# Performance work log

Measured on AMD Instinct MI355X. Metric: run time of the kernel, lower is better.

## Reference

```python
import jax, jax.numpy as jnp
import numpy as np
import math

DIM = 512
HID = 2048
BS, SLEN = 4, 4096


def _bayes_linear(x, mu, log_sigma, eps):
    # torchbnn BayesLinear: W = mu + exp(log_sigma) * eps; y = x @ W^T
    W = mu + jnp.exp(log_sigma) * eps
    return jnp.einsum('...i,oi->...o', x, W)


def setup_inputs() -> dict:
    key = jax.random.key(0)
    ks = jax.random.split(key, 20)
    d = {}
    d['x'] = jax.random.normal(ks[0], (BS, SLEN, DIM), dtype=jnp.float32)
    # causal additive mask, broadcast over batch
    causal = jnp.triu(jnp.full((SLEN, SLEN), -1e9, dtype=jnp.float32), k=1)
    d['mask'] = causal[None, :, :]
    shapes = {'wk': (DIM, DIM), 'wv': (DIM, DIM), 'wo': (DIM, DIM), 'w1': (HID, DIM), 'w2': (DIM, HID)}
    i = 1
    for name, shp in shapes.items():
        fan_in = shp[1]
        d[name + '_mu'] = jax.random.normal(ks[i], shp, dtype=jnp.float32) / np.sqrt(fan_in); i += 1
        d[name + '_ls'] = (-3.0 + 0.1 * jax.random.normal(ks[i], shp, dtype=jnp.float32)); i += 1
        d[name + '_eps'] = jax.random.normal(ks[i], shp, dtype=jnp.float32); i += 1
    return d


def reference(x, mask, wk_mu, wk_ls, wk_eps, wv_mu, wv_ls, wv_eps, wo_mu, wo_ls, wo_eps,
              w1_mu, w1_ls, w1_eps, w2_mu, w2_ls, w2_eps):
    dim = x.shape[-1]
    # attention: W_q is identity
    xq = x
    xk = _bayes_linear(x, wk_mu, wk_ls, wk_eps)
    xv = _bayes_linear(x, wv_mu, wv_ls, wv_eps)
    scores = jnp.einsum('bqd,bkd->bqk', xq, xk) / math.sqrt(dim) + mask
    attn = jax.nn.softmax(scores, axis=-1)
    h = jnp.einsum('bqk,bkd->bqd', attn, xv)
    h_attn = _bayes_linear(h, wo_mu, wo_ls, wo_eps)
    h_res = x + h_attn
    # FFN with ReLU
    ff = _bayes_linear(h_res, w1_mu, w1_ls, w1_eps)
    ff = jax.nn.relu(ff)
    ff = _bayes_linear(ff, w2_mu, w2_ls, w2_eps)
    return h_res + ff
```

## Files before the change

kernel.cpp:

```cpp
#include <hip/hip_runtime.h>
#include <hip/hip_bf16.h>

typedef __hip_bfloat16 bf16;
typedef __attribute__((ext_vector_type(8))) short short8;
typedef __attribute__((ext_vector_type(4))) float f32x4;

#define MFMA16(a,b,c) __builtin_amdgcn_mfma_f32_16x16x32_bf16(a,b,c,0,0,0)

__device__ __forceinline__ void gl_lds16(const void* g, void* l) {
  __builtin_amdgcn_global_load_lds(
      (const __attribute__((address_space(1))) void*)g,
      (__attribute__((address_space(3))) void*)l, 16, 0, 0);
}

__global__ __launch_bounds__(256) void prep_kernel(
    const float* __restrict__ x,
    const float* __restrict__ m0, const float* __restrict__ l0, const float* __restrict__ e0,
    const float* __restrict__ m1, const float* __restrict__ l1, const float* __restrict__ e1,
    const float* __restrict__ m2, const float* __restrict__ l2, const float* __restrict__ e2,
    const float* __restrict__ m3, const float* __restrict__ l3, const float* __restrict__ e3,
    const float* __restrict__ m4, const float* __restrict__ l4, const float* __restrict__ e4,
    bf16* __restrict__ xb, bf16* __restrict__ wts)
{
  long e = ((long)blockIdx.x * 256 + threadIdx.x) * 4;
  if (e < 8388608L) {
    float4 v = *(const float4*)(x + e);
    union { bf16 b[4]; short4 s; } u;
    u.b[0] = __float2bfloat16(v.x); u.b[1] = __float2bfloat16(v.y);
    u.b[2] = __float2bfloat16(v.z); u.b[3] = __float2bfloat16(v.w);
    *(short4*)(xb + e) = u.s;
  } else {
    long we = e - 8388608L;
    const float *mu, *ls, *ep; long off = we;
    if (we < 262144L)        { mu = m0; ls = l0; ep = e0; }
    else if (we < 524288L)   { mu = m1; ls = l1; ep = e1; off = we - 262144L; }
    else if (we < 786432L)   { mu = m2; ls = l2; ep = e2; off = we - 524288L; }
    else if (we < 1835008L)  { mu = m3; ls = l3; ep = e3; off = we - 786432L; }
    else                     { mu = m4; ls = l4; ep = e4; off = we - 1835008L; }
    float4 a = *(const float4*)(mu + off);
    float4 b = *(const float4*)(ls + off);
    float4 c = *(const float4*)(ep + off);
    union { bf16 w[4]; short4 s; } u;
    u.w[0] = __float2bfloat16(a.x + __expf(b.x) * c.x);
    u.w[1] = __float2bfloat16(a.y + __expf(b.y) * c.y);
    u.w[2] = __float2bfloat16(a.z + __expf(b.z) * c.z);
    u.w[3] = __float2bfloat16(a.w + __expf(b.w) * c.w);
    *(short4*)(wts + we) = u.s;
  }
}

template<int MODE>
__global__ __launch_bounds__(256, 2) void gemm_nt(
    const bf16* __restrict__ A, const bf16* __restrict__ B,
    const float* __restrict__ resid, float* __restrict__ outf,
    bf16* __restrict__ outb, int M, int N, int K)
{
  __shared__ bf16 As[128 * 64];
  __shared__ bf16 Bs[128 * 64];
  const int t = threadIdx.x, w = t >> 6, lane = t & 63;
  const int quad = lane >> 4, c16 = lane & 15;
  const int bm = blockIdx.x << 7, bn = blockIdx.y << 7;
  const int wr = (w >> 1) << 6, wc = (w & 1) << 6;

  f32x4 acc[4][4] = {};

  const int lh = lane >> 3, l8 = lane & 7;
  const int gcol = (l8 ^ lh) << 3;
  const bf16* Ab = A + (long)bm * K;
  const bf16* Bb = B + (long)bn * K;

  for (int k0 = 0; k0 < K; k0 += 64) {
    #pragma unroll
    for (int r2 = 0; r2 < 4; r2++) {
      const int R0 = r2 * 32 + w * 8;
      gl_lds16(Ab + (long)(R0 + lh) * K + k0 + gcol, (char*)As + R0 * 128);
      gl_lds16(Bb + (long)(R0 + lh) * K + k0 + gcol, (char*)Bs + R0 * 128);
    }
    __syncthreads();
    short8 a[2][4], b[2][4];
    const int sw = c16 & 7;
    #pragma unroll
    for (int i = 0; i < 4; i++) {
      const int ra = (wr + i * 16 + c16) * 64;
      const int rb = (wc + i * 16 + c16) * 64;
      a[0][i] = *(const short8*)(As + ra + ((quad ^ sw) << 3));
      a[1][i] = *(const short8*)(As + ra + (((quad + 4) ^ sw) << 3));
      b[0][i] = *(const short8*)(Bs + rb + ((quad ^ sw) << 3));
      b[1][i] = *(const short8*)(Bs + rb + (((quad + 4) ^ sw) << 3));
    }
    #pragma unroll
    for (int kk = 0; kk < 2; kk++)
      #pragma unroll
      for (int i = 0; i < 4; i++)
        #pragma unroll
        for (int j = 0; j < 4; j++)
          acc[i][j] = MFMA16(a[kk][i], b[kk][j], acc[i][j]);
    __syncthreads();
  }

  #pragma unroll
  for (int i = 0; i < 4; i++) {
    const int row = bm + wr + i * 16 + quad * 4;
    #pragma unroll
    for (int j = 0; j < 4; j++) {
      const int col = bn + wc + j * 16 + c16;
      #pragma unroll
      for (int r = 0; r < 4; r++) {
        float v = acc[i][j][r];
        if (MODE == 4) {
          int n = (row + r) & 31;
          long idx = (long)(row + r) * 512 + ((((col >> 3) ^ (n & 7)) << 3) | (col & 7));
          outb[idx] = __float2bfloat16(v);
        } else if (MODE == 5) {
          int g = row + r;
          int kvl = g & 31;
          long idx = (((long)(g >> 5)) << 14) + (long)col * 32 +
                     (((kvl >> 3) ^ ((col >> 1) & 3)) << 3) + (kvl & 7);
          outb[idx] = __float2bfloat16(v);
        } else {
          long idx = (long)(row + r) * N + col;
          if (MODE == 0) {
            outb[idx] = __float2bfloat16(v);
          } else if (MODE == 1) {
            float vv = v + resid[idx];
            outf[idx] = vv;
            outb[idx] = __float2bfloat16(vv);
          } else if (MODE == 2) {
            outb[idx] = __float2bfloat16(v > 0.f ? v : 0.f);
          } else {
            outf[idx] = v + resid[idx];
          }
        }
      }
    }
  }
}

__global__ __launch_bounds__(256, 2) void attn4_kernel(
    const bf16* __restrict__ xq, const bf16* __restrict__ xkS,
    const bf16* __restrict__ xvS, bf16* __restrict__ Opart,
    float* __restrict__ lsum)
{
  __shared__ bf16 Ks[32 * 512];
  __shared__ bf16 Vs[512 * 32];
  __shared__ bf16 Pb[4 * 512];

  const int t = threadIdx.x, w = t >> 6, lane = t & 63;
  const int quad = lane >> 4, c16 = lane & 15;
  const int n = blockIdx.x;
  const int B = n & 3, par = (n >> 2) & 3, i = n >> 4;
  const long boff = (long)B * (4096L * 512);
  const float scale = 0.04419417382415922f;
  const float FM = 30.0f;

  union { short8 s; short u[8]; } ones;
  #pragma unroll
  for (int k = 0; k < 8; k++) ones.u[k] = (short)0x3F80;

  for (int seg = 0; seg < 2; seg++) {
    const int qt = seg ? (63 - i) : i;
    const int T = 2 * (qt + 1);
    const int qb = qt << 6;

    short8 qf[16];
    {
      const bf16* qrow = xq + boff + (long)(qb + w * 16 + c16) * 512 + quad * 8;
      #pragma unroll
      for (int f = 0; f < 16; f++) qf[f] = *(const short8*)(qrow + f * 32);
    }

    f32x4 o[32];
    #pragma unroll
    for (int jj = 0; jj < 32; jj++) o[jj] = (f32x4){0.f, 0.f, 0.f, 0.f};
    f32x4 lacc = (f32x4){0.f, 0.f, 0.f, 0.f};

    for (int tile = par; tile < T; tile += 4) {
      const int kv0 = tile << 5;
      {
        const long tb = ((long)(B * 128 + tile)) << 14;
        const bf16* ks = xkS + tb + (w << 9) + (lane << 3);
        const bf16* vs = xvS + tb + (w << 9) + (lane << 3);
        char* kd = (char*)Ks + (w << 10);
        char* vd = (char*)Vs + (w << 10);
        #pragma unroll
        for (int r2 = 0; r2 < 8; r2++) {
          gl_lds16(ks + (r2 << 11), kd + (r2 << 12));
          gl_lds16(vs + (r2 << 11), vd + (r2 << 12));
        }
      }
      __syncthreads();

      f32x4 s0 = (f32x4){0.f, 0.f, 0.f, 0.f};
      f32x4 s1 = s0;
      const int n0 = c16, n1 = 16 + c16;
      const int sw0 = (c16 & 7) << 3;
      #pragma unroll
      for (int f = 0; f < 16; f++) {
        int cb = (f * 4 + quad) << 3;
        short8 b0 = *(const short8*)(Ks + n0 * 512 + (cb ^ sw0));
        short8 b1 = *(const short8*)(Ks + n1 * 512 + (cb ^ sw0));
        s0 = MFMA16(qf[f], b0, s0);
        s1 = MFMA16(qf[f], b1, s1);
      }

      bf16* Pw = Pb + (w << 9);
      {
        const int qr0 = qb + w * 16 + quad * 4;
        const bool need_mask = (kv0 + 32 > qb);
        #pragma unroll
        for (int r = 0; r < 4; r++) {
          float p0 = __expf(fmaf(s0[r], scale, -FM));
          float p1 = __expf(fmaf(s1[r], scale, -FM));
          if (need_mask) {
            if (kv0 + n0 > qr0 + r) p0 = 0.f;
            if (kv0 + n1 > qr0 + r) p1 = 0.f;
          }
          int pr = quad * 4 + r;
          int swp = (pr >> 1) & 3;
          Pw[pr * 32 + (((n0 >> 3) ^ swp) << 3) + (n0 & 7)] = __float2bfloat16(p0);
          Pw[pr * 32 + (((n1 >> 3) ^ swp) << 3) + (n1 & 7)] = __float2bfloat16(p1);
        }
      }
      short8 pa = *(const short8*)(Pw + c16 * 32 + ((quad ^ ((c16 >> 1) & 3)) << 3));
      lacc = MFMA16(pa, ones.s, lacc);
      #pragma unroll
      for (int jj = 0; jj < 32; jj++) {
        int d = jj * 16 + c16;
        short8 vb = *(const short8*)(Vs + d * 32 + ((quad ^ ((d >> 1) & 3)) << 3));
        o[jj] = MFMA16(pa, vb, o[jj]);
      }
      __syncthreads();
    }

    const int pidx = (B * 64 + qt) * 4 + par;
    {
      bf16* ob = Opart + ((long)pidx << 15) + (long)(w * 16 + quad * 4) * 512 + c16;
      #pragma unroll
      for (int r = 0; r < 4; r++) {
        #pragma unroll
        for (int jj = 0; jj < 32; jj++)
          ob[(long)r * 512 + jj * 16] = __float2bfloat16(o[jj][r]);
      }
      if (c16 == 0) {
        #pragma unroll
        for (int r = 0; r < 4; r++)
          lsum[pidx * 64 + w * 16 + quad * 4 + r] = lacc[r];
      }
    }
  }
}

__global__ __launch_bounds__(256) void combine_kernel(
    const bf16* __restrict__ Opart, const float* __restrict__ lsum,
    bf16* __restrict__ hb)
{
  const int t = threadIdx.x;
  const int r = blockIdx.x * 4 + (t >> 6);
  const int B = r >> 12, rl = r & 4095, qt = rl >> 6, rr = rl & 63;
  const int p0 = (B * 64 + qt) * 4;
  float lt = lsum[p0 * 64 + rr] + lsum[(p0 + 1) * 64 + rr] +
             lsum[(p0 + 2) * 64 + rr] + lsum[(p0 + 3) * 64 + rr];
  float inv = 1.0f / lt;
  const int d0 = (t & 63) * 8;
  union { short8 s; bf16 b[8]; } u0, u1, u2, u3, uo;
  u0.s = *(const short8*)(Opart + (((long)(p0 + 0) << 6) + rr) * 512 + d0);
  u1.s = *(const short8*)(Opart + (((long)(p0 + 1) << 6) + rr) * 512 + d0);
  u2.s = *(const short8*)(Opart + (((long)(p0 + 2) << 6) + rr) * 512 + d0);
  u3.s = *(const short8*)(Opart + (((long)(p0 + 3) << 6) + rr) * 512 + d0);
  #pragma unroll
  for (int k = 0; k < 8; k++) {
    float s = __bfloat162float(u0.b[k]) + __bfloat162float(u1.b[k]) +
              __bfloat162float(u2.b[k]) + __bfloat162float(u3.b[k]);
    uo.b[k] = __float2bfloat16(s * inv);
  }
  *(short8*)(hb + (long)r * 512 + d0) = uo.s;
}

extern "C" void kernel_launch(void* const* d_in, const int* in_sizes, int n_in,
                              void* d_out, int out_size, void* d_ws, size_t ws_size,
                              hipStream_t stream) {
  (void)in_sizes; (void)n_in; (void)out_size; (void)ws_size;
  const float* x = (const float*)d_in[0];
  const float* wk_mu = (const float*)d_in[2],  *wk_ls = (const float*)d_in[3],  *wk_eps = (const float*)d_in[4];
  const float* wv_mu = (const float*)d_in[5],  *wv_ls = (const float*)d_in[6],  *wv_eps = (const float*)d_in[7];
  const float* wo_mu = (const float*)d_in[8],  *wo_ls = (const float*)d_in[9],  *wo_eps = (const float*)d_in[10];
  const float* w1_mu = (const float*)d_in[11], *w1_ls = (const float*)d_in[12], *w1_eps = (const float*)d_in[13];
  const float* w2_mu = (const float*)d_in[14], *w2_ls = (const float*)d_in[15], *w2_eps = (const float*)d_in[16];

  const long MB = 1048576L;
  char* ws = (char*)d_ws;
  bf16*   xb    = (bf16*)(ws + 0);
  bf16*   xkS   = (bf16*)(ws + 16 * MB);
  bf16*   xvS   = (bf16*)(ws + 32 * MB);
  bf16*   Opart = (bf16*)(ws + 48 * MB);
  float*  lsb   = (float*)(ws + 112 * MB);
  bf16*   wts   = (bf16*)(ws + 113 * MB);
  bf16*   hb    = (bf16*)(ws + 32 * MB);
  float*  hrf   = (float*)(ws + 64 * MB);
  bf16*   hrb   = (bf16*)(ws + 96 * MB);
  bf16*   ffb   = (bf16*)(ws + 0);

  bf16* wkb = wts;
  bf16* wvb = wts + 262144;
  bf16* wob = wts + 524288;
  bf16* w1b = wts + 786432;
  bf16* w2b = wts + 1835008;

  prep_kernel<<<11008, 256, 0, stream>>>(x,
      wk_mu, wk_ls, wk_eps, wv_mu, wv_ls, wv_eps, wo_mu, wo_ls, wo_eps,
      w1_mu, w1_ls, w1_eps, w2_mu, w2_ls, w2_eps, xb, wts);

  gemm_nt<4><<<dim3(128, 4),  256, 0, stream>>>(xb,  wkb, nullptr, nullptr, xkS, 16384, 512, 512);
  gemm_nt<5><<<dim3(128, 4),  256, 0, stream>>>(xb,  wvb, nullptr, nullptr, xvS, 16384, 512, 512);

  attn4_kernel<<<512, 256, 0, stream>>>(xb, xkS, xvS, Opart, lsb);
  combine_kernel<<<4096, 256, 0, stream>>>(Opart, lsb, hb);

  gemm_nt<1><<<dim3(128, 4),  256, 0, stream>>>(hb,  wob, x,   hrf, hrb, 16384, 512, 512);
  gemm_nt<2><<<dim3(128, 16), 256, 0, stream>>>(hrb, w1b, nullptr, nullptr, ffb, 16384, 2048, 512);
  gemm_nt<3><<<dim3(128, 4),  256, 0, stream>>>(ffb, w2b, hrf, (float*)d_out, nullptr, 16384, 512, 2048);
}
```

Measured before the change: 464.8 us.

## Fuse K/V projections, drop fp32 residual buffer, add nontemporal stores, raise occupancy

Merges the K and V projection GEMMs into one launch over a concatenated 1024-wide weight, relying on wk and wv sitting next to each other in the weight buffer and xkS/xvS being 8M elements apart. Stops writing the fp32 h_res buffer and instead reads the residual back as bf16 in the final GEMM, which cuts traffic but loses precision on the residual path. Adds nontemporal stores and loads for the ReLU output, the attention partials and the combine reads. It also splits the GEMM fragment loads per k-step and raises launch bounds to 3 waves to lower register pressure and allow more resident blocks.

```diff
diff --git a/kernel.cpp b/kernel.cpp
--- a/kernel.cpp
+++ b/kernel.cpp
@@ -11,6 +11,10 @@
   __builtin_amdgcn_global_load_lds(
       (const __attribute__((address_space(1))) void*)g,
       (__attribute__((address_space(3))) void*)l, 16, 0, 0);
+}
+
+__device__ __forceinline__ void nt_store_bf16(bf16* p, bf16 v) {
+  __builtin_nontemporal_store(*(short*)&v, (short*)p);
 }
 
 __global__ __launch_bounds__(256) void prep_kernel(
@@ -50,10 +54,10 @@
 }
 
 template<int MODE>
-__global__ __launch_bounds__(256, 2) void gemm_nt(
+__global__ __launch_bounds__(256, 3) void gemm_nt(
     const bf16* __restrict__ A, const bf16* __restrict__ B,
-    const float* __restrict__ resid, float* __restrict__ outf,
-    bf16* __restrict__ outb, int M, int N, int K)
+    const float* __restrict__ residf, const bf16* __restrict__ residb,
+    float* __restrict__ outf, bf16* __restrict__ outb, int M, int N, int K)
 {
   __shared__ bf16 As[128 * 64];
   __shared__ bf16 Bs[128 * 64];
@@ -77,24 +81,21 @@
       gl_lds16(Bb + (long)(R0 + lh) * K + k0 + gcol, (char*)Bs + R0 * 128);
     }
     __syncthreads();
-    short8 a[2][4], b[2][4];
     const int sw = c16 & 7;
     #pragma unroll
-    for (int i = 0; i < 4; i++) {
-      const int ra = (wr + i * 16 + c16) * 64;
-      const int rb = (wc + i * 16 + c16) * 64;
-      a[0][i] = *(const short8*)(As + ra + ((quad ^ sw) << 3));
-      a[1][i] = *(const short8*)(As + ra + (((quad + 4) ^ sw) << 3));
-      b[0][i] = *(const short8*)(Bs + rb + ((quad ^ sw) << 3));
-      b[1][i] = *(const short8*)(Bs + rb + (((quad + 4) ^ sw) << 3));
-    }
-    #pragma unroll
-    for (int kk = 0; kk < 2; kk++)
+    for (int kk = 0; kk < 2; kk++) {
+      short8 a[4], b[4];
+      #pragma unroll
+      for (int i = 0; i < 4; i++) {
+        a[i] = *(const short8*)(As + (wr + i * 16 + c16) * 64 + (((kk * 4 + quad) ^ sw) << 3));
+        b[i] = *(const short8*)(Bs + (wc + i * 16 + c16) * 64 + (((kk * 4 + quad) ^ sw) << 3));
+      }
       #pragma unroll
       for (int i = 0; i < 4; i++)
         #pragma unroll
         for (int j = 0; j < 4; j++)
-          acc[i][j] = MFMA16(a[kk][i], b[kk][j], acc[i][j]);
+          acc[i][j] = MFMA16(a[i], b[j], acc[i][j]);
+    }
     __syncthreads();
   }
 
@@ -107,28 +108,27 @@
       #pragma unroll
       for (int r = 0; r < 4; r++) {
         float v = acc[i][j][r];
-        if (MODE == 4) {
-          int n = (row + r) & 31;
-          long idx = (long)(row + r) * 512 + ((((col >> 3) ^ (n & 7)) << 3) | (col & 7));
-          outb[idx] = __float2bfloat16(v);
-        } else if (MODE == 5) {
-          int g = row + r;
-          int kvl = g & 31;
-          long idx = (((long)(g >> 5)) << 14) + (long)col * 32 +
-                     (((kvl >> 3) ^ ((col >> 1) & 3)) << 3) + (kvl & 7);
-          outb[idx] = __float2bfloat16(v);
+        if (MODE == 6) {
+          const int g = row + r;
+          if (col < 512) {
+            int n = g & 31;
+            long idx = (long)g * 512 + ((((col >> 3) ^ (n & 7)) << 3) | (col & 7));
+            outb[idx] = __float2bfloat16(v);
+          } else {
+            int c = col - 512;
+            int kvl = g & 31;
+            long idx = (((long)(g >> 5)) << 14) + (long)c * 32 +
+                       (((kvl >> 3) ^ ((c >> 1) & 3)) << 3) + (kvl & 7);
+            outb[(1L << 23) + idx] = __float2bfloat16(v);
+          }
         } else {
           long idx = (long)(row + r) * N + col;
-          if (MODE == 0) {
-            outb[idx] = __float2bfloat16(v);
-          } else if (MODE == 1) {
-            float vv = v + resid[idx];
-            outf[idx] = vv;
-            outb[idx] = __float2bfloat16(vv);
+          if (MODE == 1) {
+            outb[idx] = __float2bfloat16(v + residf[idx]);
           } else if (MODE == 2) {
-            outb[idx] = __float2bfloat16(v > 0.f ? v : 0.f);
-          } else {
-            outf[idx] = v + resid[idx];
+            nt_store_bf16(outb + idx, __float2bfloat16(v > 0.f ? v : 0.f));
+          } else if (MODE == 3) {
+            __builtin_nontemporal_store(v + __bfloat162float(residb[idx]), outf + idx);
           }
         }
       }
@@ -239,7 +239,7 @@
       for (int r = 0; r < 4; r++) {
         #pragma unroll
         for (int jj = 0; jj < 32; jj++)
-          ob[(long)r * 512 + jj * 16] = __float2bfloat16(o[jj][r]);
+          nt_store_bf16(ob + (long)r * 512 + jj * 16, __float2bfloat16(o[jj][r]));
       }
       if (c16 == 0) {
         #pragma unroll
@@ -263,10 +263,10 @@
   float inv = 1.0f / lt;
   const int d0 = (t & 63) * 8;
   union { short8 s; bf16 b[8]; } u0, u1, u2, u3, uo;
-  u0.s = *(const short8*)(Opart + (((long)(p0 + 0) << 6) + rr) * 512 + d0);
-  u1.s = *(const short8*)(Opart + (((long)(p0 + 1) << 6) + rr) * 512 + d0);
-  u2.s = *(const short8*)(Opart + (((long)(p0 + 2) << 6) + rr) * 512 + d0);
-  u3.s = *(const short8*)(Opart + (((long)(p0 + 3) << 6) + rr) * 512 + d0);
+  u0.s = __builtin_nontemporal_load((const short8*)(Opart + (((long)(p0 + 0) << 6) + rr) * 512 + d0));
+  u1.s = __builtin_nontemporal_load((const short8*)(Opart + (((long)(p0 + 1) << 6) + rr) * 512 + d0));
+  u2.s = __builtin_nontemporal_load((const short8*)(Opart + (((long)(p0 + 2) << 6) + rr) * 512 + d0));
+  u3.s = __builtin_nontemporal_load((const short8*)(Opart + (((long)(p0 + 3) << 6) + rr) * 512 + d0));
   #pragma unroll
   for (int k = 0; k < 8; k++) {
     float s = __bfloat162float(u0.b[k]) + __bfloat162float(u1.b[k]) +
@@ -296,12 +296,10 @@
   float*  lsb   = (float*)(ws + 112 * MB);
   bf16*   wts   = (bf16*)(ws + 113 * MB);
   bf16*   hb    = (bf16*)(ws + 32 * MB);
-  float*  hrf   = (float*)(ws + 64 * MB);
-  bf16*   hrb   = (bf16*)(ws + 96 * MB);
+  bf16*   hrb   = (bf16*)(ws + 64 * MB);
   bf16*   ffb   = (bf16*)(ws + 0);
 
   bf16* wkb = wts;
-  bf16* wvb = wts + 262144;
   bf16* wob = wts + 524288;
   bf16* w1b = wts + 786432;
   bf16* w2b = wts + 1835008;
@@ -310,13 +308,12 @@
       wk_mu, wk_ls, wk_eps, wv_mu, wv_ls, wv_eps, wo_mu, wo_ls, wo_eps,
       w1_mu, w1_ls, w1_eps, w2_mu, w2_ls, w2_eps, xb, wts);
 
-  gemm_nt<4><<<dim3(128, 4),  256, 0, stream>>>(xb,  wkb, nullptr, nullptr, xkS, 16384, 512, 512);
-  gemm_nt<5><<<dim3(128, 4),  256, 0, stream>>>(xb,  wvb, nullptr, nullptr, xvS, 16384, 512, 512);
+  gemm_nt<6><<<dim3(128, 8),  256, 0, stream>>>(xb, wkb, nullptr, nullptr, nullptr, xkS, 16384, 1024, 512);
 
   attn4_kernel<<<512, 256, 0, stream>>>(xb, xkS, xvS, Opart, lsb);
   combine_kernel<<<4096, 256, 0, stream>>>(Opart, lsb, hb);
 
-  gemm_nt<1><<<dim3(128, 4),  256, 0, stream>>>(hb,  wob, x,   hrf, hrb, 16384, 512, 512);
-  gemm_nt<2><<<dim3(128, 16), 256, 0, stream>>>(hrb, w1b, nullptr, nullptr, ffb, 16384, 2048, 512);
-  gemm_nt<3><<<dim3(128, 4),  256, 0, stream>>>(ffb, w2b, hrf, (float*)d_out, nullptr, 16384, 512, 2048);
-}
+  gemm_nt<1><<<dim3(128, 4),  256, 0, stream>>>(hb,  wob, x, nullptr, nullptr, hrb, 16384, 512, 512);
+  gemm_nt<2><<<dim3(128, 16), 256, 0, stream>>>(hrb, w1b, nullptr, nullptr, nullptr, ffb, 16384, 2048, 512);
+  gemm_nt<3><<<dim3(128, 4),  256, 0, stream>>>(ffb, w2b, nullptr, hrb, (float*)d_out, nullptr, 16384, 512, 2048);
+}
```

Result: slower. 511.8 us (+10.1%).
